# Kernel tuning notes

Hardware: AMD Instinct MI355X
Metric: run time of the kernel (lower is better)

## Reference

```python
import jax, jax.numpy as jnp
import numpy as np
from jax.scipy.special import i0

B, P = 2, 524288
N = (512, 512)            # uniform frequency grid
M = 4                     # window cutoff m (2M taps per dim)
SIGMA = 2.0
NGRID = tuple(2 * (int(SIGMA * Ni) // 2) for Ni in N)  # oversampled grid (1024, 1024)
BETA = tuple(float(np.pi * (2.0 - 1.0 / (ng / Ni))) for ng, Ni in zip(NGRID, N))


def _phi_hat_1d(Ni, ni, b):
    # Fourier coefficients of the Kaiser-Bessel window, k = -Ni/2 .. Ni/2-1
    k = jnp.arange(-Ni // 2, Ni // 2, dtype=jnp.float32)
    arg = jnp.sqrt(b * b - (2.0 * jnp.pi * k / ni) ** 2)
    return i0(M * arg) / ni


def _window_ft():
    # separable d-dim Fourier coefficient grid, shape [N1, N2] (== window.ft)
    c1 = _phi_hat_1d(N[0], NGRID[0], BETA[0])
    c2 = _phi_hat_1d(N[1], NGRID[1], BETA[1])
    return c1[:, None] * c2[None, :]


def _phi(t, ni, b):
    # Kaiser-Bessel window in time domain, support |t| <= M/ni
    u2 = M * M - (ni * t) ** 2
    u = jnp.sqrt(jnp.maximum(u2, 1e-12))
    return jnp.where(u2 > 0, jnp.sinh(b * u) / (jnp.pi * u), 0.0)


def setup_inputs() -> dict:
    key = jax.random.key(0)
    k1, k2 = jax.random.split(key)
    x = jax.random.uniform(k1, (B, P, 2), jnp.float32, -0.5, 0.5)  # points on torus
    f_hat = jax.random.normal(k2, (B, N[0], N[1], 2), jnp.float32)  # complex as [re,im]
    return {"x": x, "f_hat": f_hat}


def _nfft_forward(x, f_hat):
    # f(x_j) ~= sum_k f_hat[k] exp(-2 pi i <k, x_j>) via window-deconvolved oversampled FFT + local gather
    fh = (f_hat[..., 0] + 1j * f_hat[..., 1]).astype(jnp.complex64)  # [B, N1, N2]
    ft = _window_ft().astype(jnp.float32)
    gh = fh / ft                                                    # deconvolve
    p1 = (NGRID[0] - N[0]) // 2
    p2 = (NGRID[1] - N[1]) // 2
    gh = jnp.pad(gh, ((0, 0), (p1, p1), (p2, p2)))                  # centered zero-pad to n
    g = jnp.fft.fftn(jnp.fft.ifftshift(gh, axes=(-2, -1)), axes=(-2, -1))
    g = g / (NGRID[0] * NGRID[1])                                   # g_l = (1/n) sum_k gh_k e^{-2pi i kl/n}

    offs = jnp.arange(-M + 1, M + 1)                                # [2M]
    ws, idxs = [], []
    for d in range(2):
        nd = NGRID[d]
        xd = x[..., d]                                              # [B, P]
        l0 = jnp.floor(xd * nd).astype(jnp.int32)
        l = l0[..., None] + offs                                    # [B, P, 2M]
        t = xd[..., None] - l.astype(jnp.float32) / nd
        ws.append(_phi(t, nd, BETA[d]))
        idxs.append(jnp.mod(l, nd))

    g_flat = g.reshape(B, NGRID[0] * NGRID[1])
    acc = jnp.zeros((B, P), jnp.complex64)
    for i in range(2 * M):                                          # fixed 2m x 2m taps
        for j in range(2 * M):
            flat = idxs[0][..., i] * NGRID[1] + idxs[1][..., j]     # [B, P]
            gv = jnp.take_along_axis(g_flat, flat, axis=1)
            acc = acc + (ws[0][..., i] * ws[1][..., j]) * gv
    return jnp.stack([acc.real, acc.imag], axis=-1)                 # [B, P, 2]


def reference(x, f_hat):
    return _nfft_forward(x, f_hat)
```

## Files before the change

kernel.cpp:

```cpp
#include <hip/hip_runtime.h>

constexpr int   NGRID = 1024;
constexpr int   BATCH = 2;
constexpr int   NPTS  = 524288;
constexpr int   BINS  = 2048;
constexpr int   CAP   = 768;
constexpr float BETA  = 4.71238898038469f;
constexpr float PI_F  = 3.14159265358979f;

#define PIDX(i) ((i) + ((i) >> 4))

constexpr size_t G_BYTES  = (size_t)BATCH * NGRID * NGRID * sizeof(float2);
constexpr size_t GCNT_OFF = G_BYTES;
constexpr size_t PERM_OFF = G_BYTES + 8192;

__device__ __forceinline__ float i0f_large(float x) {
    float t = 3.75f / x;
    float p =  0.00392377f;
    p = p * t + -0.01647633f;
    p = p * t +  0.02635537f;
    p = p * t + -0.02057706f;
    p = p * t +  0.00916281f;
    p = p * t + -0.00157565f;
    p = p * t +  0.00225319f;
    p = p * t +  0.01328592f;
    p = p * t +  0.39894228f;
    return __expf(x) * rsqrtf(x) * p;
}

__device__ __forceinline__ int tile_of(float2 xv, int b) {
    int c1 = ((int)floorf(xv.x * 1024.0f)) & 1023;
    int c2 = ((int)floorf(xv.y * 1024.0f)) & 1023;
    return (b << 10) + ((c1 >> 5) << 5) + (c2 >> 5);
}

__device__ __forceinline__ float2 cmul(float2 a, float2 w) {
    return make_float2(a.x * w.x - a.y * w.y, a.x * w.y + a.y * w.x);
}

__device__ __forceinline__ int digitrev4_10(int f) {
    unsigned r = __brev((unsigned)f) >> 22;
    return (int)(((r & 0x2AAu) >> 1) | ((r & 0x155u) << 1));
}

__device__ __forceinline__ void build_tw4(float2* T, int tid, int nthreads) {
    int off = 0, q = 256, sig = 1;
    #pragma unroll
    for (int st = 0; st < 5; ++st) {
        for (int m = tid; m < 3 * q; m += nthreads) {
            int sec = 0, j = m;
            if (j >= q) { sec++; j -= q; }
            if (j >= q) { sec++; j -= q; }
            float ang = (-2.0f * PI_F / 1024.0f) * (float)((sec + 1) * j * sig);
            float sw, cw;
            __sincosf(ang, &sw, &cw);
            T[off + m] = make_float2(cw, sw);
        }
        off += 3 * q; q >>= 2; sig <<= 2;
    }
}

__device__ __forceinline__ void bfly4(float2* s, const float2* T,
                                      int bt, int q, int off) {
    int j    = bt & (q - 1);
    int base = ((bt - j) << 2) + j;
    int p0 = PIDX(base), p1 = PIDX(base + q);
    int p2 = PIDX(base + 2 * q), p3 = PIDX(base + 3 * q);
    float2 a0 = s[p0], a1 = s[p1], a2 = s[p2], a3 = s[p3];
    float2 t0 = make_float2(a0.x + a2.x, a0.y + a2.y);
    float2 t1 = make_float2(a0.x - a2.x, a0.y - a2.y);
    float2 t2 = make_float2(a1.x + a3.x, a1.y + a3.y);
    float2 t3 = make_float2(a1.x - a3.x, a1.y - a3.y);
    float2 b0 = make_float2(t0.x + t2.x, t0.y + t2.y);
    float2 b2 = make_float2(t0.x - t2.x, t0.y - t2.y);
    float2 b1 = make_float2(t1.x + t3.y, t1.y - t3.x);
    float2 b3 = make_float2(t1.x - t3.y, t1.y + t3.x);
    s[p0] = b0;
    s[p1] = cmul(b1, T[off + j]);
    s[p2] = cmul(b2, T[off + q + j]);
    s[p3] = cmul(b3, T[off + 2 * q + j]);
}

__global__ __launch_bounds__(256) void rows_and_bin(const float2* __restrict__ fh,
                                                    float2* __restrict__ g,
                                                    const float2* __restrict__ x,
                                                    int* __restrict__ gcnt,
                                                    int* __restrict__ perm) {
    __shared__ __align__(16) char smem[16880];
    int tid = threadIdx.x;

    if (blockIdx.x < 1024) {
        float2* s = (float2*)smem;
        float2* T = (float2*)smem + 1087;
        int blk = blockIdx.x & 511;
        int b   = blockIdx.x >> 9;
        int row = (blk < 256) ? blk : blk + 512;
        int a1  = (row + 256) & 1023;

        build_tw4(T, tid, 256);

        float k1 = (float)(a1 - 256);
        float w1 = (2.0f * PI_F / 1024.0f) * k1;
        float c1 = i0f_large(4.0f * sqrtf(BETA * BETA - w1 * w1));

        const float2* fr = fh + ((long)b << 18) + ((long)a1 << 9);

        float w2a = (2.0f * PI_F / 1024.0f) * (float)tid;
        float c2a = i0f_large(4.0f * sqrtf(BETA * BETA - w2a * w2a));
        float w2b = (2.0f * PI_F / 1024.0f) * (float)(tid - 256);
        float c2b = i0f_large(4.0f * sqrtf(BETA * BETA - w2b * w2b));

        float2 va = fr[tid + 256];
        float2 vb = fr[tid];
        float ia = 1.0f / (c1 * c2a);
        float ib = 1.0f / (c1 * c2b);
        float2 A = make_float2(va.x * ia, va.y * ia);
        float2 B = make_float2(vb.x * ib, vb.y * ib);

        __syncthreads();

        s[PIDX(tid)]       = make_float2(A.x + B.x, A.y + B.y);
        s[PIDX(tid + 256)] = cmul(make_float2(A.x - B.y, A.y + B.x), T[tid]);
        s[PIDX(tid + 512)] = cmul(make_float2(A.x - B.x, A.y - B.y), T[256 + tid]);
        s[PIDX(tid + 768)] = cmul(make_float2(A.x + B.y, A.y - B.x), T[512 + tid]);

        int off = 768, q = 64;
        #pragma unroll
        for (int st = 0; st < 4; ++st) {
            __syncthreads();
            bfly4(s, T, tid, q, off);
            off += 3 * q; q >>= 2;
        }
        __syncthreads();

        float2* base = g + ((long)b << 20) + ((long)row << 10);
        #pragma unroll
        for (int i = 0; i < 4; ++i) {
            int idx = tid + (i << 8);
            base[idx] = s[PIDX(digitrev4_10(idx))];
        }
    } else {
        int* h = (int*)smem;
        int bblk = blockIdx.x - 1024;
        for (int i = tid; i < BINS; i += 256) h[i] = 0;
        __syncthreads();

        int base = bblk * 4096;
        int tile[16];
        #pragma unroll
        for (int i = 0; i < 16; ++i) {
            int gid = base + tid + i * 256;
            tile[i] = tile_of(x[gid], gid >> 19);
            atomicAdd(&h[tile[i]], 1);
        }
        __syncthreads();

        #pragma unroll
        for (int j = 0; j < 8; ++j) {
            int bi = tid + j * 256;
            int c  = h[bi];
            h[bi]  = c ? atomicAdd(&gcnt[bi], c) : 0;
        }
        __syncthreads();

        #pragma unroll
        for (int i = 0; i < 16; ++i) {
            int pos = atomicAdd(&h[tile[i]], 1);
            perm[tile[i] * CAP + pos] = base + tid + i * 256;
        }
    }
}

__global__ __launch_bounds__(256) void fft_cols(float2* __restrict__ g) {
    constexpr int STR = 1092;
    __shared__ float2 s[4 * STR];
    __shared__ float2 T[1023];
    int b  = blockIdx.y;
    int C0 = blockIdx.x * 4;
    int t  = threadIdx.x;
    int c  = t & 3, L = t >> 2;
    float2* gb = g + ((long)b << 20);

    build_tw4(T, t, 256);

    float2 E[16];
    #pragma unroll
    for (int m = 0; m < 4; ++m) {
        int r = L + 64 * m;
        E[m] = gb[((long)r << 10) + C0 + c];
    }
    #pragma unroll
    for (int m = 12; m < 16; ++m) {
        int r = L + 64 * m;
        E[m] = gb[((long)r << 10) + C0 + c];
    }
    __syncthreads();

    #pragma unroll
    for (int m = 0; m < 4; ++m) {
        float2 A = E[m], B = E[m + 12];
        int j = L + 64 * m;
        E[m]      = make_float2(A.x + B.x, A.y + B.y);
        E[m + 4]  = cmul(make_float2(A.x - B.y, A.y + B.x), T[j]);
        E[m + 8]  = cmul(make_float2(A.x - B.x, A.y - B.y), T[256 + j]);
        E[m + 12] = cmul(make_float2(A.x + B.y, A.y - B.x), T[512 + j]);
    }

    {
        float2 u1 = T[768 + L], u2 = T[768 + 64 + L], u3 = T[768 + 128 + L];
        #pragma unroll
        for (int a = 0; a < 4; ++a) {
            float2 a0 = E[4*a], a1 = E[4*a+1], a2 = E[4*a+2], a3 = E[4*a+3];
            float2 t0 = make_float2(a0.x + a2.x, a0.y + a2.y);
            float2 t1 = make_float2(a0.x - a2.x, a0.y - a2.y);
            float2 t2 = make_float2(a1.x + a3.x, a1.y + a3.y);
            float2 t3 = make_float2(a1.x - a3.x, a1.y - a3.y);
            E[4*a]   = make_float2(t0.x + t2.x, t0.y + t2.y);
            E[4*a+1] = cmul(make_float2(t1.x + t3.y, t1.y - t3.x), u1);
            E[4*a+2] = cmul(make_float2(t0.x - t2.x, t0.y - t2.y), u2);
            E[4*a+3] = cmul(make_float2(t1.x - t3.y, t1.y + t3.x), u3);
        }
    }

    float2* sf = s + c * STR;
    #pragma unroll
    for (int m = 0; m < 16; ++m) sf[PIDX(L + 64 * m)] = E[m];

    int off = 960, q = 16;
    #pragma unroll
    for (int st = 0; st < 3; ++st) {
        __syncthreads();
        #pragma unroll
        for (int rr = 0; rr < 4; ++rr)
            bfly4(sf, T, L + rr * 64, q, off);
        off += 3 * q; q >>= 2;
    }
    __syncthreads();

    #pragma unroll
    for (int i = 0; i < 16; ++i) {
        int r = L + i * 64;
        gb[((long)r << 10) + C0 + c] = sf[PIDX(digitrev4_10(r))];
    }
}

__global__ __launch_bounds__(256) void gather_binned(const float2* __restrict__ x,
                                                     const float2* __restrict__ g,
                                                     const int* __restrict__ gcnt,
                                                     const int* __restrict__ perm,
                                                     float2* __restrict__ out) {
    __shared__ float2 patch[37 * 37];
    __shared__ float2 W[6 * 128];
    int tb = blockIdx.x;
    int b  = tb >> 10;
    int tt = tb & 1023;
    int tR = tt >> 5, tC = tt & 31;
    int R0 = (tR << 5) - 2, C0 = (tC << 5) - 2;
    const float2* gb = g + ((long)b << 20);

    for (int p = threadIdx.x; p < 37 * 37; p += 256) {
        int pr = p / 37, pc = p - pr * 37;
        int gr = (R0 + pr) & 1023, gc = (C0 + pc) & 1023;
        patch[p] = gb[(gr << 10) + gc];
    }
    for (int e = threadIdx.x; e < 768; e += 256) {
        int k = e >> 7, i = e & 127;
        float t0 = (float)i * 0.0078125f - (float)(k - 2);
        float t1 = t0 + 0.0078125f;
        float u20 = 16.0f - t0 * t0, u21 = 16.0f - t1 * t1;
        float ir0 = rsqrtf(u20),     ir1 = rsqrtf(u21);
        float v0 = __expf(BETA * u20 * ir0) * 0.159154943f * ir0;
        float v1 = __expf(BETA * u21 * ir1) * 0.159154943f * ir1;
        W[e] = make_float2(v0, v1 - v0);
    }
    __syncthreads();

    int cnt = gcnt[tb];
    if (cnt > CAP) cnt = CAP;
    int off0 = tb * CAP;
    for (int i = (int)threadIdx.x; i < cnt; i += 256) {
        int gid = perm[off0 + i];
        float2 xv = x[gid];

        float w1[6], w2[6];
        int rr0, cc0;
        {
            float xs = xv.x * 1024.0f;
            float fl = floorf(xs);
            float fr = xs - fl;
            rr0 = (((int)fl) & 1023) - (tR << 5);
            float fi = fr * 128.0f;
            int   ti = (int)fi;
            float fc = fi - (float)ti;
            #pragma unroll
            for (int k = 0; k < 6; ++k) {
                float2 wd = W[(k << 7) + ti];
                w1[k] = fmaf(fc, wd.y, wd.x);
            }
        }
        {
            float xs = xv.y * 1024.0f;
            float fl = floorf(xs);
            float fr = xs - fl;
            cc0 = (((int)fl) & 1023) - (tC << 5);
            float fi = fr * 128.0f;
            int   ti = (int)fi;
            float fc = fi - (float)ti;
            #pragma unroll
            for (int k = 0; k < 6; ++k) {
                float2 wd = W[(k << 7) + ti];
                w2[k] = fmaf(fc, wd.y, wd.x);
            }
        }

        float ar = 0.0f, ai = 0.0f;
        #pragma unroll
        for (int ii = 0; ii < 6; ++ii) {
            int pbase = (rr0 + ii) * 37 + cc0;
            float wi = w1[ii];
            #pragma unroll
            for (int jj = 0; jj < 6; ++jj) {
                float2 gv = patch[pbase + jj];
                float w = wi * w2[jj];
                ar = fmaf(w, gv.x, ar);
                ai = fmaf(w, gv.y, ai);
            }
        }
        out[gid] = make_float2(ar, ai);
    }
}

extern "C" void kernel_launch(void* const* d_in, const int* in_sizes, int n_in,
                              void* d_out, int out_size, void* d_ws, size_t ws_size,
                              hipStream_t stream) {
    const float2* x  = (const float2*)d_in[0];
    const float2* fh = (const float2*)d_in[1];
    char* ws = (char*)d_ws;
    float2* g   = (float2*)ws;
    int* gcnt   = (int*)(ws + GCNT_OFF);
    int* perm   = (int*)(ws + PERM_OFF);

    hipMemsetAsync(gcnt, 0, BINS * sizeof(int), stream);

    rows_and_bin<<<dim3(1280), dim3(256), 0, stream>>>(fh, g, x, gcnt, perm);
    fft_cols    <<<dim3(256, BATCH), dim3(256), 0, stream>>>(g);

    gather_binned<<<dim3(BINS), dim3(256), 0, stream>>>(x, g, gcnt, perm, (float2*)d_out);
}
```

Before: 128.1 us.

## Store point coordinates in binned records and compute window weights directly

The binning pass now writes a float4 record (x, y, index) per point instead of just the index. The gather kernel no longer does a dependent random read of x through the permutation. The gather kernel also drops its per-block shared-memory lookup table and interpolation and evaluates the Kaiser-Bessel weights directly with rsqrt/exp per tap. This removes an indirect global load and a table-setup phase, but quadruples the perm write/read traffic and adds transcendental math per point.

```diff
diff --git a/kernel.cpp b/kernel.cpp
--- a/kernel.cpp
+++ b/kernel.cpp
@@ -85,7 +85,7 @@
                                                     float2* __restrict__ g,
                                                     const float2* __restrict__ x,
                                                     int* __restrict__ gcnt,
-                                                    int* __restrict__ perm) {
+                                                    float4* __restrict__ perm) {
     __shared__ __align__(16) char smem[16880];
     int tid = threadIdx.x;
 
@@ -146,11 +146,13 @@
         __syncthreads();
 
         int base = bblk * 4096;
-        int tile[16];
+        int    tile[16];
+        float2 pv[16];
         #pragma unroll
         for (int i = 0; i < 16; ++i) {
             int gid = base + tid + i * 256;
-            tile[i] = tile_of(x[gid], gid >> 19);
+            pv[i]   = x[gid];
+            tile[i] = tile_of(pv[i], gid >> 19);
             atomicAdd(&h[tile[i]], 1);
         }
         __syncthreads();
@@ -165,8 +167,10 @@
 
         #pragma unroll
         for (int i = 0; i < 16; ++i) {
+            int gid = base + tid + i * 256;
             int pos = atomicAdd(&h[tile[i]], 1);
-            perm[tile[i] * CAP + pos] = base + tid + i * 256;
+            perm[tile[i] * CAP + pos] =
+                make_float4(pv[i].x, pv[i].y, __int_as_float(gid), 0.0f);
         }
     }
 }
@@ -244,13 +248,11 @@
     }
 }
 
-__global__ __launch_bounds__(256) void gather_binned(const float2* __restrict__ x,
-                                                     const float2* __restrict__ g,
+__global__ __launch_bounds__(256) void gather_binned(const float2* __restrict__ g,
                                                      const int* __restrict__ gcnt,
-                                                     const int* __restrict__ perm,
+                                                     const float4* __restrict__ perm,
                                                      float2* __restrict__ out) {
     __shared__ float2 patch[37 * 37];
-    __shared__ float2 W[6 * 128];
     int tb = blockIdx.x;
     int b  = tb >> 10;
     int tt = tb & 1023;
@@ -263,53 +265,43 @@
         int gr = (R0 + pr) & 1023, gc = (C0 + pc) & 1023;
         patch[p] = gb[(gr << 10) + gc];
     }
-    for (int e = threadIdx.x; e < 768; e += 256) {
-        int k = e >> 7, i = e & 127;
-        float t0 = (float)i * 0.0078125f - (float)(k - 2);
-        float t1 = t0 + 0.0078125f;
-        float u20 = 16.0f - t0 * t0, u21 = 16.0f - t1 * t1;
-        float ir0 = rsqrtf(u20),     ir1 = rsqrtf(u21);
-        float v0 = __expf(BETA * u20 * ir0) * 0.159154943f * ir0;
-        float v1 = __expf(BETA * u21 * ir1) * 0.159154943f * ir1;
-        W[e] = make_float2(v0, v1 - v0);
-    }
     __syncthreads();
 
     int cnt = gcnt[tb];
     if (cnt > CAP) cnt = CAP;
     int off0 = tb * CAP;
     for (int i = (int)threadIdx.x; i < cnt; i += 256) {
-        int gid = perm[off0 + i];
-        float2 xv = x[gid];
+        float4 rec = perm[off0 + i];
+        int gid = __float_as_int(rec.z);
 
         float w1[6], w2[6];
         int rr0, cc0;
         {
-            float xs = xv.x * 1024.0f;
+            float xs = rec.x * 1024.0f;
             float fl = floorf(xs);
             float fr = xs - fl;
             rr0 = (((int)fl) & 1023) - (tR << 5);
-            float fi = fr * 128.0f;
-            int   ti = (int)fi;
-            float fc = fi - (float)ti;
             #pragma unroll
             for (int k = 0; k < 6; ++k) {
-                float2 wd = W[(k << 7) + ti];
-                w1[k] = fmaf(fc, wd.y, wd.x);
+                float tv = fr - (float)(k - 2);
+                float u2 = 16.0f - tv * tv;
+                float ir = rsqrtf(u2);
+                float z  = BETA * u2 * ir;
+                w1[k] = __expf(z) * 0.159154943f * ir;
             }
         }
         {
-            float xs = xv.y * 1024.0f;
+            float xs = rec.y * 1024.0f;
             float fl = floorf(xs);
             float fr = xs - fl;
             cc0 = (((int)fl) & 1023) - (tC << 5);
-            float fi = fr * 128.0f;
-            int   ti = (int)fi;
-            float fc = fi - (float)ti;
             #pragma unroll
             for (int k = 0; k < 6; ++k) {
-                float2 wd = W[(k << 7) + ti];
-                w2[k] = fmaf(fc, wd.y, wd.x);
+                float tv = fr - (float)(k - 2);
+                float u2 = 16.0f - tv * tv;
+                float ir = rsqrtf(u2);
+                float z  = BETA * u2 * ir;
+                w2[k] = __expf(z) * 0.159154943f * ir;
             }
         }
 
@@ -336,14 +328,14 @@
     const float2* x  = (const float2*)d_in[0];
     const float2* fh = (const float2*)d_in[1];
     char* ws = (char*)d_ws;
-    float2* g   = (float2*)ws;
-    int* gcnt   = (int*)(ws + GCNT_OFF);
-    int* perm   = (int*)(ws + PERM_OFF);
+    float2* g    = (float2*)ws;
+    int*    gcnt = (int*)(ws + GCNT_OFF);
+    float4* perm = (float4*)(ws + PERM_OFF);
 
     hipMemsetAsync(gcnt, 0, BINS * sizeof(int), stream);
 
     rows_and_bin<<<dim3(1280), dim3(256), 0, stream>>>(fh, g, x, gcnt, perm);
     fft_cols    <<<dim3(256, BATCH), dim3(256), 0, stream>>>(g);
 
-    gather_binned<<<dim3(BINS), dim3(256), 0, stream>>>(x, g, gcnt, perm, (float2*)d_out);
-}
+    gather_binned<<<dim3(BINS), dim3(256), 0, stream>>>(g, gcnt, perm, (float2*)d_out);
+}
```

After: 118.6 us. 7.4% less time.
